# Kernel optimization log

Measured on AMD Instinct MI355X. Metric: run time of the kernel, lower is better.

The kernel has to match this reference:

```python
import jax, jax.numpy as jnp
import numpy as np

N_NODES = 50000
N_EDGES = 800000
IN_CH = 128
EDGE_DIM = 16
N_GRAPHS = 500


def _lin_params(key, din, dout):
    k1, k2 = jax.random.split(key)
    s = 1.0 / np.sqrt(din)
    W = jax.random.uniform(k1, (din, dout), jnp.float32, -s, s)
    b = jax.random.uniform(k2, (dout,), jnp.float32, -s, s)
    return W, b


def setup_inputs() -> dict:
    key = jax.random.key(0)
    ks = jax.random.split(key, 20)
    x = jax.random.normal(ks[0], (N_NODES, IN_CH), jnp.float32)
    edge_attr = jax.random.normal(ks[1], (N_EDGES, EDGE_DIM), jnp.float32)
    edge_index = jax.random.randint(ks[2], (2, N_EDGES), 0, N_NODES, jnp.int32)
    n_nodes = jnp.full((N_GRAPHS,), N_NODES // N_GRAPHS, jnp.int32)
    inp = {"x": x, "edge_attr": edge_attr, "edge_index": edge_index, "n_nodes": n_nodes}
    # conv1: edge lin (edge_dim->128), mlp 128->256->256, bn 256
    inp["We1"], inp["be1"] = _lin_params(ks[3], EDGE_DIM, IN_CH)
    inp["W11"], inp["b11"] = _lin_params(ks[4], IN_CH, 256)
    inp["W12"], inp["b12"] = _lin_params(ks[5], 256, 256)
    inp["g1"], inp["bt1"] = jnp.ones((256,), jnp.float32), jnp.zeros((256,), jnp.float32)
    # conv2: edge lin (edge_dim->256), mlp 256->128->128, bn 128
    inp["We2"], inp["be2"] = _lin_params(ks[6], EDGE_DIM, 256)
    inp["W21"], inp["b21"] = _lin_params(ks[7], 256, 128)
    inp["W22"], inp["b22"] = _lin_params(ks[8], 128, 128)
    inp["g2"], inp["bt2"] = jnp.ones((128,), jnp.float32), jnp.zeros((128,), jnp.float32)
    # conv3: edge lin (edge_dim->128), mlp 128->64->64, bn 64
    inp["We3"], inp["be3"] = _lin_params(ks[9], EDGE_DIM, 128)
    inp["W31"], inp["b31"] = _lin_params(ks[10], 128, 64)
    inp["W32"], inp["b32"] = _lin_params(ks[11], 64, 64)
    inp["g3"], inp["bt3"] = jnp.ones((64,), jnp.float32), jnp.zeros((64,), jnp.float32)
    # head
    inp["Wf1"], inp["bf1"] = _lin_params(ks[12], 64, 16)
    inp["Wf2"], inp["bf2"] = _lin_params(ks[13], 16, 1)
    return inp


def _gine(x, src, dst, ea_proj, W1, b1, W2, b2):
    # message: relu(x_j + lin(edge_attr)); aggregate: scatter-add; GIN0 eps=0
    m = jax.nn.relu(x[src] + ea_proj)                      # [E, D]
    agg = jax.ops.segment_sum(m, dst, num_segments=N_NODES)
    h = x + agg
    return jax.nn.relu(h @ W1 + b1) @ W2 + b2


def _bn(x, g, b):
    mu = x.mean(axis=0)
    var = x.var(axis=0)
    return (x - mu) * jax.lax.rsqrt(var + 1e-5) * g + b


def reference(x, edge_attr, edge_index, n_nodes,
              We1, be1, W11, b11, W12, b12, g1, bt1,
              We2, be2, W21, b21, W22, b22, g2, bt2,
              We3, be3, W31, b31, W32, b32, g3, bt3,
              Wf1, bf1, Wf2, bf2):
    src, dst = edge_index[0], edge_index[1]
    h = _gine(x, src, dst, edge_attr @ We1 + be1, W11, b11, W12, b12)
    h = _bn(jax.nn.relu(h), g1, bt1)
    h = _gine(h, src, dst, edge_attr @ We2 + be2, W21, b21, W22, b22)
    h = _bn(jax.nn.relu(h), g2, bt2)
    h = _gine(h, src, dst, edge_attr @ We3 + be3, W31, b31, W32, b32)
    h = _bn(jax.nn.relu(h), g3, bt3)
    last_idx = jnp.cumsum(n_nodes) - 1                      # [G]
    master = h[last_idx]                                    # [G, 64]; dropout = identity (eval)
    out = jax.nn.relu(master @ Wf1 + bf1) @ Wf2 + bf2       # [G, 1]
    return out
```

## Files before the change

### kernel.cpp

```cpp
#include <hip/hip_runtime.h>
#include <hip/hip_bf16.h>


typedef __attribute__((ext_vector_type(8))) short short8;
typedef __attribute__((ext_vector_type(4))) float floatx4;
typedef __attribute__((ext_vector_type(2))) float float2v;

__device__ __forceinline__ float2v splat2(float s) {
    float2v v; v[0] = s; v[1] = s; return v;
}

__device__ __forceinline__ ushort f2bf_rne(float x) {
    unsigned u = __float_as_uint(x);
    unsigned r = (u + 0x7FFFu + ((u >> 16) & 1u)) >> 16;
    return (ushort)r;
}

__device__ __forceinline__ float bf2f(ushort u) {
    return __uint_as_float(((unsigned)u) << 16);
}


__global__ __launch_bounds__(256) void hist_kernel(const int* __restrict__ dst,
                                                   int* __restrict__ deg, int E) {
    int i = blockIdx.x * blockDim.x + threadIdx.x;
    int stride = gridDim.x * blockDim.x;
    for (; i < E; i += stride) atomicAdd(&deg[dst[i]], 1);
}

__global__ __launch_bounds__(1024) void scan_kernel(const int* __restrict__ deg,
                                                    int* __restrict__ row_start, int N) {
    __shared__ int part[1024];
    int tid = threadIdx.x;
    int per = (N + 1023) / 1024;
    int start = tid * per;
    int end = min(start + per, N);
    int s = 0;
    for (int i = start; i < end; ++i) s += deg[i];
    part[tid] = s;
    __syncthreads();
    if (tid == 0) {
        int t = 0;
        for (int i = 0; i < 1024; ++i) {
            int v = part[i];
            part[i] = t;
            t += v;
        }
    }
    __syncthreads();
    int run = part[tid];
    for (int i = start; i < end; ++i) {
        row_start[i] = run;
        run += deg[i];
    }
    if (tid == 1023) row_start[N] = run;
}

__global__ __launch_bounds__(256) void scatter_kernel(
    const int* __restrict__ src, const int* __restrict__ dst,
    const int* __restrict__ row_start, int* __restrict__ cursor,
    int* __restrict__ csr_eid, int* __restrict__ csr_src, int E) {
    int i = blockIdx.x * blockDim.x + threadIdx.x;
    int stride = gridDim.x * blockDim.x;
    for (; i < E; i += stride) {
        int v = dst[i];
        int p = row_start[v] + atomicAdd(&cursor[v], 1);
        csr_eid[p] = i;
        csr_src[p] = src[i];
    }
}

__device__ __forceinline__ void wsplit(const float* W, ushort* Wth, ushort* Wtl,
                                       int K, int N, int t) {
    int k = t / N, n = t - k * N;
    float v = W[t];
    ushort hv = f2bf_rne(v);
    float hf = bf2f(hv);
    ushort lv = f2bf_rne(v - hf);
    Wth[(size_t)n * K + k] = hv;
    Wtl[(size_t)n * K + k] = lv;
}

__global__ __launch_bounds__(256) void prep_all(
    const float* W11, ushort* W11h, ushort* W11l,
    const float* W12, ushort* W12h, ushort* W12l,
    const float* W21, ushort* W21h, ushort* W21l,
    const float* W22, ushort* W22h, ushort* W22l,
    const float* W31, ushort* W31h, ushort* W31l,
    const float* W32, ushort* W32h, ushort* W32l) {
    int t = blockIdx.x * blockDim.x + threadIdx.x;
    const int s1 = 128 * 256, s2 = s1 + 256 * 256, s3 = s2 + 256 * 128;
    const int s4 = s3 + 128 * 128, s5 = s4 + 128 * 64, s6 = s5 + 64 * 64;
    if (t < s1) wsplit(W11, W11h, W11l, 128, 256, t);
    else if (t < s2) wsplit(W12, W12h, W12l, 256, 256, t - s1);
    else if (t < s3) wsplit(W21, W21h, W21l, 256, 128, t - s2);
    else if (t < s4) wsplit(W22, W22h, W22l, 128, 128, t - s3);
    else if (t < s5) wsplit(W31, W31h, W31l, 128, 64, t - s4);
    else if (t < s6) wsplit(W32, W32h, W32l, 64, 64, t - s5);
}

__global__ __launch_bounds__(256) void f32_to_bf16(const float* __restrict__ in,
                                                   ushort* __restrict__ out, long n4) {
    long i = (long)blockIdx.x * blockDim.x + threadIdx.x;
    long stride = (long)gridDim.x * blockDim.x;
    for (; i < n4; i += stride) {
        float4 v = ((const float4*)in)[i];
        ushort4 o;
        o.x = f2bf_rne(v.x);
        o.y = f2bf_rne(v.y);
        o.z = f2bf_rne(v.z);
        o.w = f2bf_rne(v.w);
        ((ushort4*)out)[i] = o;
    }
}

template <int D>
__global__ __launch_bounds__(256) void gine_agg_kernel(
    const float* __restrict__ h, const ushort* __restrict__ hb,
    const float* __restrict__ ea,
    const int* __restrict__ row_start, const int* __restrict__ csr_eid,
    const int* __restrict__ csr_src,
    const float* __restrict__ We, const float* __restrict__ be,
    ushort* __restrict__ uhi, ushort* __restrict__ ulo, int N) {
    constexpr int CPL = D / 64;
    constexpr int C2 = CPL / 2;
    const int lane = threadIdx.x & 63;
    const int ch0 = lane * CPL;

    float2v w[16][C2];
#pragma unroll
    for (int k = 0; k < 16; ++k)
#pragma unroll
        for (int c = 0; c < C2; ++c)
            w[k][c] = *(const float2v*)&We[k * D + ch0 + 2 * c];
    float2v bias[C2];
#pragma unroll
    for (int c = 0; c < C2; ++c) bias[c] = *(const float2v*)&be[ch0 + 2 * c];

    int v = blockIdx.x * 4 + (threadIdx.x >> 6);
    const int vstride = gridDim.x * 4;
    const float2v z2 = splat2(0.f);

    for (; v < N; v += vstride) {
        const int e0 = row_start[v];
        const int e1 = row_start[v + 1];
        float2v acc[C2];
#pragma unroll
        for (int c = 0; c < C2; ++c) acc[c] = z2;

        int i = e0;
        for (; i + 8 <= e1; i += 8) {
            int myeid = csr_eid[i + (lane >> 3)];
            float2v eav = *(const float2v*)&ea[(size_t)myeid * 16 + (lane & 7) * 2];
            float2v hv[8][C2];
#pragma unroll
            for (int j = 0; j < 8; ++j) {
                int s = csr_src[i + j];
                if (CPL == 4) {
                    ushort4 r = *(const ushort4*)&hb[(size_t)s * D + ch0];
                    hv[j][0][0] = bf2f(r.x);
                    hv[j][0][1] = bf2f(r.y);
                    hv[j][C2 - 1][0] = bf2f(r.z);
                    hv[j][C2 - 1][1] = bf2f(r.w);
                } else {
                    ushort2 r = *(const ushort2*)&hb[(size_t)s * D + ch0];
                    hv[j][0][0] = bf2f(r.x);
                    hv[j][0][1] = bf2f(r.y);
                }
            }
#pragma unroll
            for (int j = 0; j < 8; ++j) {
                float wk[16];
#pragma unroll
                for (int k = 0; k < 16; ++k)
                    wk[k] = __int_as_float(__builtin_amdgcn_readlane(
                        __float_as_int(eav[k & 1]), j * 8 + (k >> 1)));
#pragma unroll
                for (int c = 0; c < C2; ++c) {
                    float2v p = bias[c];
#pragma unroll
                    for (int k = 0; k < 16; ++k)
                        p = __builtin_elementwise_fma(splat2(wk[k]), w[k][c], p);
                    float2v m = p + hv[j][c];
                    acc[c] += __builtin_elementwise_max(m, z2);
                }
            }
        }
        if (i < e1) {
            int eclamp = e1 - 1;
            int myeid = csr_eid[min(i + (lane >> 3), eclamp)];
            float2v eav = *(const float2v*)&ea[(size_t)myeid * 16 + (lane & 7) * 2];
#pragma unroll
            for (int j = 0; j < 8; ++j) {
                if (i + j < e1) {
                    int s = csr_src[i + j];
                    float2v hv[C2];
                    if (CPL == 4) {
                        ushort4 r = *(const ushort4*)&hb[(size_t)s * D + ch0];
                        hv[0][0] = bf2f(r.x);
                        hv[0][1] = bf2f(r.y);
                        hv[C2 - 1][0] = bf2f(r.z);
                        hv[C2 - 1][1] = bf2f(r.w);
                    } else {
                        ushort2 r = *(const ushort2*)&hb[(size_t)s * D + ch0];
                        hv[0][0] = bf2f(r.x);
                        hv[0][1] = bf2f(r.y);
                    }
                    float wk[16];
#pragma unroll
                    for (int k = 0; k < 16; ++k)
                        wk[k] = __int_as_float(__builtin_amdgcn_readlane(
                            __float_as_int(eav[k & 1]), j * 8 + (k >> 1)));
#pragma unroll
                    for (int c = 0; c < C2; ++c) {
                        float2v p = bias[c];
#pragma unroll
                        for (int k = 0; k < 16; ++k)
                            p = __builtin_elementwise_fma(splat2(wk[k]), w[k][c], p);
                        float2v m = p + hv[c];
                        acc[c] += __builtin_elementwise_max(m, z2);
                    }
                }
            }
        }
        ushort hi[CPL], lo[CPL];
#pragma unroll
        for (int c = 0; c < C2; ++c) {
            float2v sv = *(const float2v*)&h[(size_t)v * D + ch0 + 2 * c];
#pragma unroll
            for (int j = 0; j < 2; ++j) {
                float uv = sv[j] + acc[c][j];
                ushort hu = f2bf_rne(uv);
                ushort lu = f2bf_rne(uv - bf2f(hu));
                hi[2 * c + j] = hu;
                lo[2 * c + j] = lu;
            }
        }
        if (CPL == 4) {
            *(ushort4*)&uhi[(size_t)v * D + ch0] =
                make_ushort4(hi[0], hi[1], hi[CPL - 2], hi[CPL - 1]);
            *(ushort4*)&ulo[(size_t)v * D + ch0] =
                make_ushort4(lo[0], lo[1], lo[CPL - 2], lo[CPL - 1]);
        } else {
            *(ushort2*)&uhi[(size_t)v * D + ch0] = make_ushort2(hi[0], hi[1]);
            *(ushort2*)&ulo[(size_t)v * D + ch0] = make_ushort2(lo[0], lo[1]);
        }
    }
}

template <int WRITE_BF16, int STATS>
__global__ __launch_bounds__(256) void gemm_mfma(
    const ushort* __restrict__ Ah, const ushort* __restrict__ Al,
    const ushort* __restrict__ Bh, const ushort* __restrict__ Bl,
    const float* __restrict__ bias,
    float* __restrict__ Cf, ushort* __restrict__ Chi, ushort* __restrict__ Clo,
    float* __restrict__ stats, int Nreal,
    int N, int K, int relu) {
    __shared__ ushort sA[2][128][72];
    __shared__ ushort sB[2][64][72];
    const int tid = threadIdx.x;
    const int wave = tid >> 6, lane = tid & 63;
    const int lrow = lane & 15, lquad = lane >> 4;
    const int bm = blockIdx.y * 128;
    const int bn = blockIdx.x * 64;

    floatx4 acc[2][4];
#pragma unroll
    for (int i = 0; i < 2; ++i)
#pragma unroll
        for (int j = 0; j < 4; ++j) acc[i][j] = (floatx4)0.f;

    for (int k0 = 0; k0 < K; k0 += 64) {
        for (int s = tid; s < 1024; s += 256) {
            int row = s >> 3, c8 = (s & 7) * 8;
            size_t g = (size_t)(bm + row) * K + k0 + c8;
            *(int4*)&sA[0][row][c8] = *(const int4*)&Ah[g];
            *(int4*)&sA[1][row][c8] = *(const int4*)&Al[g];
        }
        for (int s = tid; s < 512; s += 256) {
            int row = s >> 3, c8 = (s & 7) * 8;
            size_t g = (size_t)(bn + row) * K + k0 + c8;
            *(int4*)&sB[0][row][c8] = *(const int4*)&Bh[g];
            *(int4*)&sB[1][row][c8] = *(const int4*)&Bl[g];
        }
        __syncthreads();
        const int rb = wave * 32;
#pragma unroll
        for (int kk = 0; kk < 2; ++kk) {
            int ko = kk * 32 + lquad * 8;
            short8 ah[2], al[2], bh[4], bl[4];
#pragma unroll
            for (int i = 0; i < 2; ++i) {
                ah[i] = *(const short8*)&sA[0][rb + i * 16 + lrow][ko];
                al[i] = *(const short8*)&sA[1][rb + i * 16 + lrow][ko];
            }
#pragma unroll
            for (int j = 0; j < 4; ++j) {
                bh[j] = *(const short8*)&sB[0][j * 16 + lrow][ko];
                bl[j] = *(const short8*)&sB[1][j * 16 + lrow][ko];
            }
#pragma unroll
            for (int i = 0; i < 2; ++i)
#pragma unroll
                for (int j = 0; j < 4; ++j) {
                    acc[i][j] = __builtin_amdgcn_mfma_f32_16x16x32_bf16(
                        ah[i], bh[j], acc[i][j], 0, 0, 0);
                    acc[i][j] = __builtin_amdgcn_mfma_f32_16x16x32_bf16(
                        ah[i], bl[j], acc[i][j], 0, 0, 0);
                    acc[i][j] = __builtin_amdgcn_mfma_f32_16x16x32_bf16(
                        al[i], bh[j], acc[i][j], 0, 0, 0);
                }
        }
        __syncthreads();
    }
    float sj[4] = {0.f, 0.f, 0.f, 0.f};
    float qj[4] = {0.f, 0.f, 0.f, 0.f};
#pragma unroll
    for (int i = 0; i < 2; ++i)
#pragma unroll
        for (int j = 0; j < 4; ++j) {
            int gc = bn + j * 16 + lrow;
            float bv = bias[gc];
#pragma unroll
            for (int r = 0; r < 4; ++r) {
                int gr = bm + wave * 32 + i * 16 + lquad * 4 + r;
                float v = acc[i][j][r] + bv;
                if (relu) v = fmaxf(v, 0.f);
                if (STATS && gr < Nreal) {
                    sj[j] += v;
                    qj[j] = fmaf(v, v, qj[j]);
                }
                if (WRITE_BF16) {
                    ushort hv = f2bf_rne(v);
                    ushort lv = f2bf_rne(v - bf2f(hv));
                    Chi[(size_t)gr * N + gc] = hv;
                    Clo[(size_t)gr * N + gc] = lv;
                } else {
                    Cf[(size_t)gr * N + gc] = v;
                }
            }
        }
    if (STATS) {
#pragma unroll
        for (int j = 0; j < 4; ++j) {
            float s = sj[j], q = qj[j];
            s += __shfl_xor(s, 16);
            s += __shfl_xor(s, 32);
            q += __shfl_xor(q, 16);
            q += __shfl_xor(q, 32);
            if (lquad == 0) {
                int gc = bn + j * 16 + lrow;
                atomicAdd(&stats[gc], s);
                atomicAdd(&stats[N + gc], q);
            }
        }
    }
}

__global__ __launch_bounds__(256) void bn_apply_kernel(
    const float* __restrict__ r, float* __restrict__ h,
    ushort* __restrict__ hbout,
    const float* __restrict__ sums,
    const float* __restrict__ g, const float* __restrict__ bt,
    int N, int D, int Dm1) {
    int idx = blockIdx.x * blockDim.x + threadIdx.x;
    int total4 = N * D / 4;
    int stride = gridDim.x * blockDim.x;
    float invN = 1.0f / (float)N;
    for (; idx < total4; idx += stride) {
        int c = (idx * 4) & Dm1;
        float4 s4 = *(const float4*)&sums[c];
        float4 q4 = *(const float4*)&sums[D + c];
        float4 g4 = *(const float4*)&g[c];
        float4 b4 = *(const float4*)&bt[c];
        float4 r4 = ((const float4*)r)[idx];
        float4 o;
        {
            float mu = s4.x * invN;
            float var = fmaf(-mu, mu, q4.x * invN);
            o.x = (r4.x - mu) * (rsqrtf(var + 1e-5f) * g4.x) + b4.x;
            mu = s4.y * invN;
            var = fmaf(-mu, mu, q4.y * invN);
            o.y = (r4.y - mu) * (rsqrtf(var + 1e-5f) * g4.y) + b4.y;
            mu = s4.z * invN;
            var = fmaf(-mu, mu, q4.z * invN);
            o.z = (r4.z - mu) * (rsqrtf(var + 1e-5f) * g4.z) + b4.z;
            mu = s4.w * invN;
            var = fmaf(-mu, mu, q4.w * invN);
            o.w = (r4.w - mu) * (rsqrtf(var + 1e-5f) * g4.w) + b4.w;
        }
        ((float4*)h)[idx] = o;
        if (hbout) {
            ushort4 ob;
            ob.x = f2bf_rne(o.x);
            ob.y = f2bf_rne(o.y);
            ob.z = f2bf_rne(o.z);
            ob.w = f2bf_rne(o.w);
            ((ushort4*)hbout)[idx] = ob;
        }
    }
}

__global__ void head_kernel(const float* __restrict__ h, const int* __restrict__ n_nodes,
                            const float* __restrict__ Wf1, const float* __restrict__ bf1,
                            const float* __restrict__ Wf2, const float* __restrict__ bf2,
                            float* __restrict__ out, int G) {
    int g = blockIdx.x * blockDim.x + threadIdx.x;
    if (g >= G) return;
    int s = 0;
    for (int i = 0; i <= g; ++i) s += n_nodes[i];
    const float* m = &h[(size_t)(s - 1) * 64];
    float o = bf2[0];
#pragma unroll 4
    for (int j = 0; j < 16; ++j) {
        float acc = bf1[j];
        for (int k = 0; k < 64; ++k) acc = fmaf(m[k], Wf1[k * 16 + j], acc);
        acc = fmaxf(acc, 0.f);
        o = fmaf(acc, Wf2[j], o);
    }
    out[g] = o;
}

extern "C" void kernel_launch(void* const* d_in, const int* in_sizes, int n_in,
                              void* d_out, int out_size, void* d_ws, size_t ws_size,
                              hipStream_t stream) {
    const float* x = (const float*)d_in[0];
    const float* ea = (const float*)d_in[1];
    const int* eidx = (const int*)d_in[2];
    const int* n_nodes = (const int*)d_in[3];
    const float* We1 = (const float*)d_in[4];
    const float* be1 = (const float*)d_in[5];
    const float* W11 = (const float*)d_in[6];
    const float* b11 = (const float*)d_in[7];
    const float* W12 = (const float*)d_in[8];
    const float* b12 = (const float*)d_in[9];
    const float* g1 = (const float*)d_in[10];
    const float* bt1 = (const float*)d_in[11];
    const float* We2 = (const float*)d_in[12];
    const float* be2 = (const float*)d_in[13];
    const float* W21 = (const float*)d_in[14];
    const float* b21 = (const float*)d_in[15];
    const float* W22 = (const float*)d_in[16];
    const float* b22 = (const float*)d_in[17];
    const float* g2 = (const float*)d_in[18];
    const float* bt2 = (const float*)d_in[19];
    const float* We3 = (const float*)d_in[20];
    const float* be3 = (const float*)d_in[21];
    const float* W31 = (const float*)d_in[22];
    const float* b31 = (const float*)d_in[23];
    const float* W32 = (const float*)d_in[24];
    const float* b32 = (const float*)d_in[25];
    const float* g3 = (const float*)d_in[26];
    const float* bt3 = (const float*)d_in[27];
    const float* Wf1 = (const float*)d_in[28];
    const float* bf1 = (const float*)d_in[29];
    const float* Wf2 = (const float*)d_in[30];
    const float* bf2 = (const float*)d_in[31];

    const int N = in_sizes[0] / 128;
    const int E = in_sizes[2] / 2;
    const int G = in_sizes[3];
    const int Mp = ((N + 127) / 128) * 128;
    const int* srcp = eidx;
    const int* dstp = eidx + E;

    float* H = (float*)d_ws;
    float* UR = H + (size_t)Mp * 256;
    float* TT = UR + (size_t)Mp * 256;
    float* stats1 = TT + (size_t)Mp * 256;
    float* stats2 = stats1 + 512;
    float* stats3 = stats2 + 256;
    int* deg = (int*)(stats3 + 128);
    int* cursor = deg + N;
    int* row_start = cursor + N;
    int* csr_eid = row_start + N + 1;
    int* csr_src = csr_eid + E;
    size_t woff = (size_t)(csr_src + E - (int*)d_ws);
    woff = (woff + 3) & ~(size_t)3;
    ushort* wp = (ushort*)((int*)d_ws + woff);
    ushort* W11th = wp; wp += 128 * 256;
    ushort* W11tl = wp; wp += 128 * 256;
    ushort* W12th = wp; wp += 256 * 256;
    ushort* W12tl = wp; wp += 256 * 256;
    ushort* W21th = wp; wp += 256 * 128;
    ushort* W21tl = wp; wp += 256 * 128;
    ushort* W22th = wp; wp += 128 * 128;
    ushort* W22tl = wp; wp += 128 * 128;
    ushort* W31th = wp; wp += 128 * 64;
    ushort* W31tl = wp; wp += 128 * 64;
    ushort* W32th = wp; wp += 64 * 64;
    ushort* W32tl = wp; wp += 64 * 64;

    hipMemsetAsync(stats1, 0, 896 * sizeof(float) + (size_t)2 * N * sizeof(int), stream);

    const int prepTot = 128 * 256 + 256 * 256 + 256 * 128 + 128 * 128 + 128 * 64 + 64 * 64;
    prep_all<<<(prepTot + 255) / 256, 256, 0, stream>>>(
        W11, W11th, W11tl, W12, W12th, W12tl, W21, W21th, W21tl,
        W22, W22th, W22tl, W31, W31th, W31tl, W32, W32th, W32tl);

    hist_kernel<<<3125, 256, 0, stream>>>(dstp, deg, E);
    scan_kernel<<<1, 1024, 0, stream>>>(deg, row_start, N);
    scatter_kernel<<<3125, 256, 0, stream>>>(srcp, dstp, row_start, cursor,
                                             csr_eid, csr_src, E);

    const int aggBlocks = (N + 3) / 4;
    const int gy = Mp / 128;
    float* R = UR;
    ushort* HB = (ushort*)TT;

    {
        ushort* Uhi = (ushort*)UR; ushort* Ulo = Uhi + (size_t)Mp * 128;
        ushort* Thi = (ushort*)TT; ushort* Tlo = Thi + (size_t)Mp * 256;
        f32_to_bf16<<<2048, 256, 0, stream>>>(x, HB, (long)N * 128 / 4);
        gine_agg_kernel<128><<<aggBlocks, 256, 0, stream>>>(
            x, HB, ea, row_start, csr_eid, csr_src, We1, be1, Uhi, Ulo, N);
        gemm_mfma<1, 0><<<dim3(4, gy), 256, 0, stream>>>(
            Uhi, Ulo, W11th, W11tl, b11, nullptr, Thi, Tlo, nullptr, 0, 256, 128, 1);
        gemm_mfma<0, 1><<<dim3(4, gy), 256, 0, stream>>>(
            Thi, Tlo, W12th, W12tl, b12, R, nullptr, nullptr, stats1, N, 256, 256, 1);
        bn_apply_kernel<<<2048, 256, 0, stream>>>(R, H, HB, stats1, g1, bt1, N, 256, 255);
    }

    {
        ushort* Uhi = (ushort*)UR; ushort* Ulo = Uhi + (size_t)Mp * 256;
        ushort* Thi = (ushort*)TT; ushort* Tlo = Thi + (size_t)Mp * 128;
        gine_agg_kernel<256><<<aggBlocks, 256, 0, stream>>>(
            H, HB, ea, row_start, csr_eid, csr_src, We2, be2, Uhi, Ulo, N);
        gemm_mfma<1, 0><<<dim3(2, gy), 256, 0, stream>>>(
            Uhi, Ulo, W21th, W21tl, b21, nullptr, Thi, Tlo, nullptr, 0, 128, 256, 1);
        gemm_mfma<0, 1><<<dim3(2, gy), 256, 0, stream>>>(
            Thi, Tlo, W22th, W22tl, b22, R, nullptr, nullptr, stats2, N, 128, 128, 1);
        bn_apply_kernel<<<2048, 256, 0, stream>>>(R, H, HB, stats2, g2, bt2, N, 128, 127);
    }

    {
        ushort* Uhi = (ushort*)UR; ushort* Ulo = Uhi + (size_t)Mp * 128;
        ushort* Thi = (ushort*)TT; ushort* Tlo = Thi + (size_t)Mp * 64;
        gine_agg_kernel<128><<<aggBlocks, 256, 0, stream>>>(
            H, HB, ea, row_start, csr_eid, csr_src, We3, be3, Uhi, Ulo, N);
        gemm_mfma<1, 0><<<dim3(1, gy), 256, 0, stream>>>(
            Uhi, Ulo, W31th, W31tl, b31, nullptr, Thi, Tlo, nullptr, 0, 64, 128, 1);
        gemm_mfma<0, 1><<<dim3(1, gy), 256, 0, stream>>>(
            Thi, Tlo, W32th, W32tl, b32, R, nullptr, nullptr, stats3, N, 64, 64, 1);
        bn_apply_kernel<<<2048, 256, 0, stream>>>(R, H, nullptr, stats3, g3, bt3, N, 64, 63);
    }

    head_kernel<<<(G + 255) / 256, 256, 0, stream>>>(H, n_nodes, Wf1, bf1, Wf2, bf2,
                                                     (float*)d_out, G);
}
```

Measured before the change: 1.033 ms.

## Interleave CSR arrays and split wide-channel aggregation across waves

Merges the separate csr_eid and csr_src arrays into one int2 array, so each edge's id and source come from a single load. Restructures the aggregation kernel so each wave handles 128 channels, two per lane. For D=256 two waves share a node, which halves per-wave register use for the edge weights and doubles the block count. Edges are now processed in groups of 4, with each lane loading one edge_attr scalar and source indices broadcast via readlane, plus a simple one-edge remainder loop. This trades fewer edges in flight per iteration and redundant edge-attr and CSR loads across the paired waves for lower register pressure and more parallelism.

```diff
diff --git a/kernel.cpp b/kernel.cpp
--- a/kernel.cpp
+++ b/kernel.cpp
@@ -59,14 +59,13 @@
 __global__ __launch_bounds__(256) void scatter_kernel(
     const int* __restrict__ src, const int* __restrict__ dst,
     const int* __restrict__ row_start, int* __restrict__ cursor,
-    int* __restrict__ csr_eid, int* __restrict__ csr_src, int E) {
+    int2* __restrict__ csr, int E) {
     int i = blockIdx.x * blockDim.x + threadIdx.x;
     int stride = gridDim.x * blockDim.x;
     for (; i < E; i += stride) {
         int v = dst[i];
         int p = row_start[v] + atomicAdd(&cursor[v], 1);
-        csr_eid[p] = i;
-        csr_src[p] = src[i];
+        csr[p] = make_int2(i, src[i]);
     }
 }
 
@@ -114,137 +113,92 @@
     }
 }
 
-template <int D>
+template <int D, int WPN>
 __global__ __launch_bounds__(256) void gine_agg_kernel(
     const float* __restrict__ h, const ushort* __restrict__ hb,
     const float* __restrict__ ea,
-    const int* __restrict__ row_start, const int* __restrict__ csr_eid,
-    const int* __restrict__ csr_src,
+    const int* __restrict__ row_start, const int2* __restrict__ csr,
     const float* __restrict__ We, const float* __restrict__ be,
     ushort* __restrict__ uhi, ushort* __restrict__ ulo, int N) {
-    constexpr int CPL = D / 64;
-    constexpr int C2 = CPL / 2;
+    constexpr int NPB = 4 / WPN;
     const int lane = threadIdx.x & 63;
-    const int ch0 = lane * CPL;
-
-    float2v w[16][C2];
-#pragma unroll
-    for (int k = 0; k < 16; ++k)
-#pragma unroll
-        for (int c = 0; c < C2; ++c)
-            w[k][c] = *(const float2v*)&We[k * D + ch0 + 2 * c];
-    float2v bias[C2];
-#pragma unroll
-    for (int c = 0; c < C2; ++c) bias[c] = *(const float2v*)&be[ch0 + 2 * c];
-
-    int v = blockIdx.x * 4 + (threadIdx.x >> 6);
-    const int vstride = gridDim.x * 4;
+    const int wid = threadIdx.x >> 6;
+    const int ch0 = (wid % WPN) * 128 + lane * 2;
+
+    float2v w[16];
+#pragma unroll
+    for (int k = 0; k < 16; ++k) w[k] = *(const float2v*)&We[k * D + ch0];
+    const float2v bias = *(const float2v*)&be[ch0];
+
+    int v = blockIdx.x * NPB + wid / WPN;
+    const int vstride = gridDim.x * NPB;
     const float2v z2 = splat2(0.f);
 
     for (; v < N; v += vstride) {
         const int e0 = row_start[v];
         const int e1 = row_start[v + 1];
-        float2v acc[C2];
-#pragma unroll
-        for (int c = 0; c < C2; ++c) acc[c] = z2;
+        float2v acc = z2;
 
         int i = e0;
-        for (; i + 8 <= e1; i += 8) {
-            int myeid = csr_eid[i + (lane >> 3)];
-            float2v eav = *(const float2v*)&ea[(size_t)myeid * 16 + (lane & 7) * 2];
-            float2v hv[8][C2];
-#pragma unroll
-            for (int j = 0; j < 8; ++j) {
-                int s = csr_src[i + j];
-                if (CPL == 4) {
-                    ushort4 r = *(const ushort4*)&hb[(size_t)s * D + ch0];
-                    hv[j][0][0] = bf2f(r.x);
-                    hv[j][0][1] = bf2f(r.y);
-                    hv[j][C2 - 1][0] = bf2f(r.z);
-                    hv[j][C2 - 1][1] = bf2f(r.w);
-                } else {
-                    ushort2 r = *(const ushort2*)&hb[(size_t)s * D + ch0];
-                    hv[j][0][0] = bf2f(r.x);
-                    hv[j][0][1] = bf2f(r.y);
-                }
+        for (; i + 4 <= e1; i += 4) {
+            int2 c2 = csr[i + (lane >> 4)];
+            float eav = ea[(size_t)c2.x * 16 + (lane & 15)];
+            int s0 = __builtin_amdgcn_readlane(c2.y, 0);
+            int s1 = __builtin_amdgcn_readlane(c2.y, 16);
+            int s2 = __builtin_amdgcn_readlane(c2.y, 32);
+            int s3 = __builtin_amdgcn_readlane(c2.y, 48);
+            ushort2 r0 = *(const ushort2*)&hb[(size_t)s0 * D + ch0];
+            ushort2 r1 = *(const ushort2*)&hb[(size_t)s1 * D + ch0];
+            ushort2 r2 = *(const ushort2*)&hb[(size_t)s2 * D + ch0];
+            ushort2 r3 = *(const ushort2*)&hb[(size_t)s3 * D + ch0];
+            float2v hv[4];
+            hv[0][0] = bf2f(r0.x); hv[0][1] = bf2f(r0.y);
+            hv[1][0] = bf2f(r1.x); hv[1][1] = bf2f(r1.y);
+            hv[2][0] = bf2f(r2.x); hv[2][1] = bf2f(r2.y);
+            hv[3][0] = bf2f(r3.x); hv[3][1] = bf2f(r3.y);
+#pragma unroll
+            for (int e = 0; e < 4; ++e) {
+                float wk[16];
+#pragma unroll
+                for (int k = 0; k < 16; ++k)
+                    wk[k] = __int_as_float(
+                        __builtin_amdgcn_readlane(__float_as_int(eav), e * 16 + k));
+                float2v p = bias;
+#pragma unroll
+                for (int k = 0; k < 16; ++k)
+                    p = __builtin_elementwise_fma(splat2(wk[k]), w[k], p);
+                float2v m = p + hv[e];
+                acc += __builtin_elementwise_max(m, z2);
             }
-#pragma unroll
-            for (int j = 0; j < 8; ++j) {
-                float wk[16];
-#pragma unroll
-                for (int k = 0; k < 16; ++k)
-                    wk[k] = __int_as_float(__builtin_amdgcn_readlane(
-                        __float_as_int(eav[k & 1]), j * 8 + (k >> 1)));
-#pragma unroll
-                for (int c = 0; c < C2; ++c) {
-                    float2v p = bias[c];
-#pragma unroll
-                    for (int k = 0; k < 16; ++k)
-                        p = __builtin_elementwise_fma(splat2(wk[k]), w[k][c], p);
-                    float2v m = p + hv[j][c];
-                    acc[c] += __builtin_elementwise_max(m, z2);
-                }
-            }
-        }
-        if (i < e1) {
-            int eclamp = e1 - 1;
-            int myeid = csr_eid[min(i + (lane >> 3), eclamp)];
-            float2v eav = *(const float2v*)&ea[(size_t)myeid * 16 + (lane & 7) * 2];
-#pragma unroll
-            for (int j = 0; j < 8; ++j) {
-                if (i + j < e1) {
-                    int s = csr_src[i + j];
-                    float2v hv[C2];
-                    if (CPL == 4) {
-                        ushort4 r = *(const ushort4*)&hb[(size_t)s * D + ch0];
-                        hv[0][0] = bf2f(r.x);
-                        hv[0][1] = bf2f(r.y);
-                        hv[C2 - 1][0] = bf2f(r.z);
-                        hv[C2 - 1][1] = bf2f(r.w);
-                    } else {
-                        ushort2 r = *(const ushort2*)&hb[(size_t)s * D + ch0];
-                        hv[0][0] = bf2f(r.x);
-                        hv[0][1] = bf2f(r.y);
-                    }
-                    float wk[16];
-#pragma unroll
-                    for (int k = 0; k < 16; ++k)
-                        wk[k] = __int_as_float(__builtin_amdgcn_readlane(
-                            __float_as_int(eav[k & 1]), j * 8 + (k >> 1)));
-#pragma unroll
-                    for (int c = 0; c < C2; ++c) {
-                        float2v p = bias[c];
-#pragma unroll
-                        for (int k = 0; k < 16; ++k)
-                            p = __builtin_elementwise_fma(splat2(wk[k]), w[k][c], p);
-                        float2v m = p + hv[c];
-                        acc[c] += __builtin_elementwise_max(m, z2);
-                    }
-                }
-            }
-        }
-        ushort hi[CPL], lo[CPL];
-#pragma unroll
-        for (int c = 0; c < C2; ++c) {
-            float2v sv = *(const float2v*)&h[(size_t)v * D + ch0 + 2 * c];
-#pragma unroll
-            for (int j = 0; j < 2; ++j) {
-                float uv = sv[j] + acc[c][j];
-                ushort hu = f2bf_rne(uv);
-                ushort lu = f2bf_rne(uv - bf2f(hu));
-                hi[2 * c + j] = hu;
-                lo[2 * c + j] = lu;
-            }
-        }
-        if (CPL == 4) {
-            *(ushort4*)&uhi[(size_t)v * D + ch0] =
-                make_ushort4(hi[0], hi[1], hi[CPL - 2], hi[CPL - 1]);
-            *(ushort4*)&ulo[(size_t)v * D + ch0] =
-                make_ushort4(lo[0], lo[1], lo[CPL - 2], lo[CPL - 1]);
-        } else {
-            *(ushort2*)&uhi[(size_t)v * D + ch0] = make_ushort2(hi[0], hi[1]);
-            *(ushort2*)&ulo[(size_t)v * D + ch0] = make_ushort2(lo[0], lo[1]);
-        }
+        }
+        for (; i < e1; ++i) {
+            int2 ce = csr[i];
+            float eav = (lane < 16) ? ea[(size_t)ce.x * 16 + lane] : 0.f;
+            ushort2 r = *(const ushort2*)&hb[(size_t)ce.y * D + ch0];
+            float wk[16];
+#pragma unroll
+            for (int k = 0; k < 16; ++k)
+                wk[k] = __int_as_float(
+                    __builtin_amdgcn_readlane(__float_as_int(eav), k));
+            float2v p = bias;
+#pragma unroll
+            for (int k = 0; k < 16; ++k)
+                p = __builtin_elementwise_fma(splat2(wk[k]), w[k], p);
+            float2v hv;
+            hv[0] = bf2f(r.x);
+            hv[1] = bf2f(r.y);
+            float2v m = p + hv;
+            acc += __builtin_elementwise_max(m, z2);
+        }
+        float2v sv = *(const float2v*)&h[(size_t)v * D + ch0];
+        float u0 = sv[0] + acc[0];
+        float u1 = sv[1] + acc[1];
+        ushort h0 = f2bf_rne(u0);
+        ushort h1 = f2bf_rne(u1);
+        ushort l0 = f2bf_rne(u0 - bf2f(h0));
+        ushort l1 = f2bf_rne(u1 - bf2f(h1));
+        *(ushort2*)&uhi[(size_t)v * D + ch0] = make_ushort2(h0, h1);
+        *(ushort2*)&ulo[(size_t)v * D + ch0] = make_ushort2(l0, l1);
     }
 }
 
@@ -473,9 +427,8 @@
     int* deg = (int*)(stats3 + 128);
     int* cursor = deg + N;
     int* row_start = cursor + N;
-    int* csr_eid = row_start + N + 1;
-    int* csr_src = csr_eid + E;
-    size_t woff = (size_t)(csr_src + E - (int*)d_ws);
+    int2* csr = (int2*)(row_start + N + 2);
+    size_t woff = (size_t)((int*)(csr + E) - (int*)d_ws);
     woff = (woff + 3) & ~(size_t)3;
     ushort* wp = (ushort*)((int*)d_ws + woff);
     ushort* W11th = wp; wp += 128 * 256;
@@ -500,10 +453,8 @@
 
     hist_kernel<<<3125, 256, 0, stream>>>(dstp, deg, E);
     scan_kernel<<<1, 1024, 0, stream>>>(deg, row_start, N);
-    scatter_kernel<<<3125, 256, 0, stream>>>(srcp, dstp, row_start, cursor,
-                                             csr_eid, csr_src, E);
-
-    const int aggBlocks = (N + 3) / 4;
+    scatter_kernel<<<3125, 256, 0, stream>>>(srcp, dstp, row_start, cursor, csr, E);
+
     const int gy = Mp / 128;
     float* R = UR;
     ushort* HB = (ushort*)TT;
@@ -512,8 +463,8 @@
         ushort* Uhi = (ushort*)UR; ushort* Ulo = Uhi + (size_t)Mp * 128;
         ushort* Thi = (ushort*)TT; ushort* Tlo = Thi + (size_t)Mp * 256;
         f32_to_bf16<<<2048, 256, 0, stream>>>(x, HB, (long)N * 128 / 4);
-        gine_agg_kernel<128><<<aggBlocks, 256, 0, stream>>>(
-            x, HB, ea, row_start, csr_eid, csr_src, We1, be1, Uhi, Ulo, N);
+        gine_agg_kernel<128, 1><<<(N + 3) / 4, 256, 0, stream>>>(
+            x, HB, ea, row_start, csr, We1, be1, Uhi, Ulo, N);
         gemm_mfma<1, 0><<<dim3(4, gy), 256, 0, stream>>>(
             Uhi, Ulo, W11th, W11tl, b11, nullptr, Thi, Tlo, nullptr, 0, 256, 128, 1);
         gemm_mfma<0, 1><<<dim3(4, gy), 256, 0, stream>>>(
@@ -524,8 +475,8 @@
     {
         ushort* Uhi = (ushort*)UR; ushort* Ulo = Uhi + (size_t)Mp * 256;
         ushort* Thi = (ushort*)TT; ushort* Tlo = Thi + (size_t)Mp * 128;
-        gine_agg_kernel<256><<<aggBlocks, 256, 0, stream>>>(
-            H, HB, ea, row_start, csr_eid, csr_src, We2, be2, Uhi, Ulo, N);
+        gine_agg_kernel<256, 2><<<(N + 1) / 2, 256, 0, stream>>>(
+            H, HB, ea, row_start, csr, We2, be2, Uhi, Ulo, N);
         gemm_mfma<1, 0><<<dim3(2, gy), 256, 0, stream>>>(
             Uhi, Ulo, W21th, W21tl, b21, nullptr, Thi, Tlo, nullptr, 0, 128, 256, 1);
         gemm_mfma<0, 1><<<dim3(2, gy), 256, 0, stream>>>(
@@ -536,8 +487,8 @@
     {
         ushort* Uhi = (ushort*)UR; ushort* Ulo = Uhi + (size_t)Mp * 128;
         ushort* Thi = (ushort*)TT; ushort* Tlo = Thi + (size_t)Mp * 64;
-        gine_agg_kernel<128><<<aggBlocks, 256, 0, stream>>>(
-            H, HB, ea, row_start, csr_eid, csr_src, We3, be3, Uhi, Ulo, N);
+        gine_agg_kernel<128, 1><<<(N + 3) / 4, 256, 0, stream>>>(
+            H, HB, ea, row_start, csr, We3, be3, Uhi, Ulo, N);
         gemm_mfma<1, 0><<<dim3(1, gy), 256, 0, stream>>>(
             Uhi, Ulo, W31th, W31tl, b31, nullptr, Thi, Tlo, nullptr, 0, 64, 128, 1);
         gemm_mfma<0, 1><<<dim3(1, gy), 256, 0, stream>>>(
```

After: 997.2 us. 1.04x faster.
